# Performance work log

Measured on AMD Instinct MI355X. Metric: run time of the kernel, lower is better.

The kernel has to match this reference:

```python
import jax, jax.numpy as jnp
import numpy as np

N = 100000      # nodes
E = 3200000     # edges (avg degree 32)
F_IN = 128      # num_node_features
H = 128         # hidden_channels


def gcn_conv(x, edge_index, W, b, n):
    """PyG-style GCNConv: linear transform, add self-loops, symmetric
    D^{-1/2} A D^{-1/2} normalization, scatter-add aggregation, bias."""
    h = x @ W  # [n, out]
    row, col = edge_index[0], edge_index[1]
    loop = jnp.arange(n, dtype=row.dtype)
    row = jnp.concatenate([row, loop])
    col = jnp.concatenate([col, loop])
    deg = jax.ops.segment_sum(jnp.ones(row.shape, h.dtype), col, num_segments=n)
    dinv = jnp.where(deg > 0, jax.lax.rsqrt(deg), 0.0)
    norm = dinv[row] * dinv[col]                 # [E+n]
    msg = h[row] * norm[:, None]                 # gather + scale
    out = jax.ops.segment_sum(msg, col, num_segments=n)  # scatter-add
    return out + b


def setup_inputs() -> dict:
    key = jax.random.key(0)
    ks = jax.random.split(key, 8)
    x = jax.random.normal(ks[0], (N, F_IN), jnp.float32)
    edge_index = jax.random.randint(ks[1], (2, E), 0, N, dtype=jnp.int32)
    s1 = 1.0 / np.sqrt(F_IN)
    s2 = 1.0 / np.sqrt(H)
    W1 = jax.random.normal(ks[2], (F_IN, H), jnp.float32) * s1
    b1 = jnp.zeros((H,), jnp.float32)
    W2 = jax.random.normal(ks[3], (H, H), jnp.float32) * s2
    b2 = jnp.zeros((H,), jnp.float32)
    Wl = jax.random.normal(ks[4], (H, 1), jnp.float32) * s2
    bl = jnp.zeros((1,), jnp.float32)
    return {"x": x, "edge_index": edge_index, "W1": W1, "b1": b1,
            "W2": W2, "b2": b2, "Wl": Wl, "bl": bl}


def reference(x, edge_index, W1, b1, W2, b2, Wl, bl):
    n = x.shape[0]
    h = jax.nn.relu(gcn_conv(x, edge_index, W1, b1, n))
    # dropout p=0.5 is identity in eval mode (training=False)
    h = jax.nn.relu(gcn_conv(h, edge_index, W2, b2, n))
    return jax.nn.sigmoid(h @ Wl + bl)  # [n, 1]
```

## Files before the change

kernel.cpp:

```cpp
#include <hip/hip_runtime.h>
#include <math.h>

#define FDIM 128
#define BKT_BITS 8
#define BKT_W (1 << BKT_BITS)
#define BIN_CHUNK 6272

typedef short bf16x8 __attribute__((ext_vector_type(8)));
typedef float f32x4 __attribute__((ext_vector_type(4)));
typedef float f32x2 __attribute__((ext_vector_type(2)));

union ABu { bf16x8 v; unsigned int u[4]; };
union F4u { float4 f; float a[4]; };

__device__ inline unsigned int pack_bf16x2(float a, float b) {
  unsigned int ua = __float_as_uint(a);
  unsigned int ub = __float_as_uint(b);
  ua = (ua + 0x7fffu + ((ua >> 16) & 1u)) >> 16;
  ub = (ub + 0x7fffu + ((ub >> 16) & 1u)) >> 16;
  return ua | (ub << 16);
}

__device__ inline unsigned char f32_to_fp8(float v) {
  return (unsigned char)(__builtin_amdgcn_cvt_pk_fp8_f32(v, v, 0, false) & 0xff);
}


__global__ __launch_bounds__(256)
void k_bhist(const int* __restrict__ col, int* __restrict__ gbcnt, int nE, int nb) {
  __shared__ int lds[512];
  for (int i = threadIdx.x; i < 512; i += 256) lds[i] = 0;
  __syncthreads();
  int stride = gridDim.x * blockDim.x;
  for (int e = blockIdx.x * blockDim.x + threadIdx.x; e < nE; e += stride)
    atomicAdd(&lds[col[e] >> BKT_BITS], 1);
  __syncthreads();
  for (int b = threadIdx.x; b < nb; b += 256) {
    int c = lds[b];
    if (c) atomicAdd(&gbcnt[b], c);
  }
}

__global__ __launch_bounds__(512)
void k_bscan(const int* __restrict__ gbcnt, int* __restrict__ gboff,
             int* __restrict__ gcur, int nb, int nE) {
  __shared__ int lds[512];
  int t = threadIdx.x;
  lds[t] = (t < nb) ? gbcnt[t] : 0;
  __syncthreads();
  for (int off = 1; off < 512; off <<= 1) {
    int x = (t >= off) ? lds[t - off] : 0;
    __syncthreads();
    lds[t] += x;
    __syncthreads();
  }
  if (t < nb) {
    int excl = (t == 0) ? 0 : lds[t - 1];
    gboff[t] = excl;
    gcur[t] = excl;
  }
  if (t == 0) gboff[nb] = nE;
}

__global__ __launch_bounds__(256)
void k_bin(const int* __restrict__ row, const int* __restrict__ col,
           int* __restrict__ gcur, int* __restrict__ pairs, int nE, int chunk, int nb) {
  __shared__ int bcnt[512];
  __shared__ int lcur[512];
  __shared__ int ecol[BIN_CHUNK];
  int e0 = blockIdx.x * chunk;
  int e1 = min(e0 + chunk, nE);
  int m = e1 - e0;
  for (int i = threadIdx.x; i < 512; i += 256) bcnt[i] = 0;
  for (int i = threadIdx.x; i < m; i += 256) ecol[i] = col[e0 + i];
  __syncthreads();
  for (int i = threadIdx.x; i < m; i += 256)
    atomicAdd(&bcnt[((unsigned)ecol[i]) >> BKT_BITS], 1);
  __syncthreads();
  for (int b = threadIdx.x; b < nb; b += 256) {
    int c = bcnt[b];
    lcur[b] = c ? atomicAdd(&gcur[b], c) : 0;
  }
  __syncthreads();
  for (int i = threadIdx.x; i < m; i += 256) {
    int c = ecol[i];
    int r = row[e0 + i];
    int p = atomicAdd(&lcur[((unsigned)c) >> BKT_BITS], 1);
    pairs[p] = r | ((c & (BKT_W - 1)) << 24);
  }
}

__global__ __launch_bounds__(1024)
void k_fine(const int* __restrict__ pairs, const int* __restrict__ gboff,
            int* __restrict__ srcs, int* __restrict__ offs, int* __restrict__ cnt,
            float* __restrict__ dinv, int n) {
  __shared__ int lcnt[256];
  __shared__ int lcur[256];
  int b = blockIdx.x;
  int t = threadIdx.x;
  int ebase = gboff[b];
  int eend = gboff[b + 1];
  if (t < 256) lcnt[t] = 0;
  __syncthreads();
  for (int e = ebase + t; e < eend; e += 1024)
    atomicAdd(&lcnt[((unsigned)pairs[e]) >> 24], 1);
  __syncthreads();
  int orig = (t < 256) ? lcnt[t] : 0;
  for (int off = 1; off < 256; off <<= 1) {
    int x = (t < 256 && t >= off) ? lcnt[t - off] : 0;
    __syncthreads();
    if (t < 256) lcnt[t] += x;
    __syncthreads();
  }
  if (t < 256) {
    int excl = lcnt[t] - orig;
    int v = (b << BKT_BITS) + t;
    if (v < n) {
      offs[v] = ebase + excl;
      cnt[v] = orig;
      dinv[v] = rsqrtf((float)(orig + 1));
    }
    lcur[t] = ebase + excl;
  }
  __syncthreads();
  for (int e = ebase + t; e < eend; e += 1024) {
    int pr = pairs[e];
    int p = atomicAdd(&lcur[((unsigned)pr) >> 24], 1);
    srcs[p] = pr & 0x00FFFFFF;
  }
}

#define STAGE_WT()                                                          \
  {                                                                         \
    int c = threadIdx.x & 127;                                              \
    for (int kp = (threadIdx.x >> 7); kp < 64; kp += 2) {                   \
      float w0 = W[(kp * 2) * 128 + c];                                     \
      float w1 = W[(kp * 2 + 1) * 128 + c];                                 \
      int unit = kp >> 2, dw = kp & 3;                                      \
      wlds[c * 64 + ((unit ^ (c & 15)) << 2) + dw] = pack_bf16x2(w0, w1);   \
    }                                                                       \
  }                                                                         \
  __syncthreads();

#define GEMM_BODY()                                                         \
  int l = threadIdx.x & 63;                                                 \
  int grp = l >> 4, c15 = l & 15;                                           \
  int rbase = blockIdx.x * 64 + (threadIdx.x >> 6) * 16;                    \
  F4u dv;                                                                   \
  dv.f = *(const float4*)(dinv + rbase + grp * 4);                          \
  f32x4 acc[8];                                                             \
  _Pragma("unroll")                                                         \
  for (int nt = 0; nt < 8; ++nt) acc[nt] = (f32x4){0.f, 0.f, 0.f, 0.f};    \
  _Pragma("unroll")                                                         \
  for (int nt = 0; nt < 8; ++nt) {                                          \
    _Pragma("unroll")                                                       \
    for (int ks = 0; ks < 4; ++ks) {                                        \
      ABu b;                                                                \
      b.v = *(const bf16x8*)&wlds[(nt * 16 + c15) * 64 +                    \
                                  ((((ks << 2) + grp) ^ c15) << 2)];        \
      acc[nt] = __builtin_amdgcn_mfma_f32_16x16x32_bf16(a[ks].v, b.v,       \
                                                        acc[nt], 0, 0, 0);  \
    }                                                                       \
  }                                                                         \
  _Pragma("unroll")                                                         \
  for (int nt = 0; nt < 8; ++nt) {                                          \
    _Pragma("unroll")                                                       \
    for (int i = 0; i < 4; ++i) {                                           \
      int r = rbase + grp * 4 + i;                                          \
      if (r < n) {                                                          \
        float v = acc[nt][i] * dv.a[i];                                     \
        out[(size_t)r * 128 + nt * 16 + c15] = f32_to_fp8(v);               \
      }                                                                     \
    }                                                                       \
  }

__global__ __launch_bounds__(256)
void k_gemm_mfma_f(const float* __restrict__ in, const float* __restrict__ W,
                   const float* __restrict__ dinv, unsigned char* __restrict__ out,
                   int n) {
  __shared__ unsigned int wlds[128 * 64];
  STAGE_WT();
  {
    int l0 = threadIdx.x & 63;
    int row = blockIdx.x * 64 + (threadIdx.x >> 6) * 16 + (l0 & 15);
    int rowc = min(row, n - 1);
    int grp0 = l0 >> 4;
    const float4* xr = (const float4*)(in + (size_t)rowc * 128);
    ABu a[4];
#pragma unroll
    for (int ks = 0; ks < 4; ++ks) {
      float4 f0 = xr[ks * 8 + grp0 * 2];
      float4 f1 = xr[ks * 8 + grp0 * 2 + 1];
      a[ks].u[0] = pack_bf16x2(f0.x, f0.y);
      a[ks].u[1] = pack_bf16x2(f0.z, f0.w);
      a[ks].u[2] = pack_bf16x2(f1.x, f1.y);
      a[ks].u[3] = pack_bf16x2(f1.z, f1.w);
    }
    GEMM_BODY();
  }
}

__global__ __launch_bounds__(256)
void k_gemm_mfma_b(const unsigned int* __restrict__ in, const float* __restrict__ W,
                   const float* __restrict__ dinv, unsigned char* __restrict__ out,
                   int n) {
  __shared__ unsigned int wlds[128 * 64];
  STAGE_WT();
  {
    int l0 = threadIdx.x & 63;
    int row = blockIdx.x * 64 + (threadIdx.x >> 6) * 16 + (l0 & 15);
    int rowc = min(row, n - 1);
    int grp0 = l0 >> 4;
    const unsigned int* hr = in + (size_t)rowc * 64;
    ABu a[4];
#pragma unroll
    for (int ks = 0; ks < 4; ++ks)
      a[ks].v = *(const bf16x8*)&hr[ks * 16 + grp0 * 4];
    GEMM_BODY();
  }
}

__device__ inline float4 agg_core(const unsigned int* __restrict__ s4,
                                  const int* __restrict__ offs,
                                  const int* __restrict__ cnt,
                                  const int* __restrict__ srcs,
                                  int v, int lane) {
  int cl = lane & 31;
  int hf = lane >> 5;
  float4 acc = make_float4(0.f, 0.f, 0.f, 0.f);
  if (lane < 32) {
    unsigned int q = s4[(size_t)v * 32 + cl];
    f32x2 lo = __builtin_amdgcn_cvt_pk_f32_fp8((int)q, false);
    f32x2 hi = __builtin_amdgcn_cvt_pk_f32_fp8((int)q, true);
    acc = make_float4(lo[0], lo[1], hi[0], hi[1]);
  }
  int beg = offs[v];
  int m = cnt[v];
  for (int base = 0; base < m; base += 64) {
    int take = m - base;
    if (take > 64) take = 64;
    int idx = (lane < take) ? srcs[beg + base + lane] : 0;
    int it = 0;
    for (; it + 7 < take; it += 8) {
      int u0 = __shfl(idx, it + hf, 64);
      int u1 = __shfl(idx, it + 2 + hf, 64);
      int u2 = __shfl(idx, it + 4 + hf, 64);
      int u3 = __shfl(idx, it + 6 + hf, 64);
      unsigned int q0 = s4[(size_t)u0 * 32 + cl];
      unsigned int q1 = s4[(size_t)u1 * 32 + cl];
      unsigned int q2 = s4[(size_t)u2 * 32 + cl];
      unsigned int q3 = s4[(size_t)u3 * 32 + cl];
      f32x2 l0 = __builtin_amdgcn_cvt_pk_f32_fp8((int)q0, false);
      f32x2 h0 = __builtin_amdgcn_cvt_pk_f32_fp8((int)q0, true);
      f32x2 l1 = __builtin_amdgcn_cvt_pk_f32_fp8((int)q1, false);
      f32x2 h1 = __builtin_amdgcn_cvt_pk_f32_fp8((int)q1, true);
      f32x2 l2 = __builtin_amdgcn_cvt_pk_f32_fp8((int)q2, false);
      f32x2 h2 = __builtin_amdgcn_cvt_pk_f32_fp8((int)q2, true);
      f32x2 l3 = __builtin_amdgcn_cvt_pk_f32_fp8((int)q3, false);
      f32x2 h3 = __builtin_amdgcn_cvt_pk_f32_fp8((int)q3, true);
      acc.x += (l0[0] + l1[0]) + (l2[0] + l3[0]);
      acc.y += (l0[1] + l1[1]) + (l2[1] + l3[1]);
      acc.z += (h0[0] + h1[0]) + (h2[0] + h3[0]);
      acc.w += (h0[1] + h1[1]) + (h2[1] + h3[1]);
    }
    for (; it + 1 < take; it += 2) {
      int u = __shfl(idx, it + hf, 64);
      unsigned int q = s4[(size_t)u * 32 + cl];
      f32x2 lo = __builtin_amdgcn_cvt_pk_f32_fp8((int)q, false);
      f32x2 hi = __builtin_amdgcn_cvt_pk_f32_fp8((int)q, true);
      acc.x += lo[0]; acc.y += lo[1]; acc.z += hi[0]; acc.w += hi[1];
    }
    if (it < take) {
      int u = __shfl(idx, it, 64);
      if (lane < 32) {
        unsigned int q = s4[(size_t)u * 32 + cl];
        f32x2 lo = __builtin_amdgcn_cvt_pk_f32_fp8((int)q, false);
        f32x2 hi = __builtin_amdgcn_cvt_pk_f32_fp8((int)q, true);
        acc.x += lo[0]; acc.y += lo[1]; acc.z += hi[0]; acc.w += hi[1];
      }
    }
  }
  acc.x += __shfl_xor(acc.x, 32, 64);
  acc.y += __shfl_xor(acc.y, 32, 64);
  acc.z += __shfl_xor(acc.z, 32, 64);
  acc.w += __shfl_xor(acc.w, 32, 64);
  return acc;
}

__global__ __launch_bounds__(256)
void k_agg_mid(const unsigned int* __restrict__ s4, const int* __restrict__ offs,
               const int* __restrict__ cnt, const int* __restrict__ srcs,
               const float* __restrict__ dinv, const float* __restrict__ bias,
               unsigned int* __restrict__ hb, int n) {
  int v = (int)(((size_t)blockIdx.x * blockDim.x + threadIdx.x) >> 6);
  if (v >= n) return;
  int lane = threadIdx.x & 63;
  float4 acc = agg_core(s4, offs, cnt, srcs, v, lane);
  if (lane < 32) {
    int cl = lane;
    float d = dinv[v];
    float4 bb = ((const float4*)bias)[cl];
    float r0 = fmaxf(acc.x * d + bb.x, 0.0f);
    float r1 = fmaxf(acc.y * d + bb.y, 0.0f);
    float r2 = fmaxf(acc.z * d + bb.z, 0.0f);
    float r3 = fmaxf(acc.w * d + bb.w, 0.0f);
    uint2 pk;
    pk.x = pack_bf16x2(r0, r1);
    pk.y = pack_bf16x2(r2, r3);
    ((uint2*)hb)[(size_t)v * 32 + cl] = pk;
  }
}

__global__ __launch_bounds__(256)
void k_agg_head(const unsigned int* __restrict__ s4, const int* __restrict__ offs,
                const int* __restrict__ cnt, const int* __restrict__ srcs,
                const float* __restrict__ dinv, const float* __restrict__ bias,
                const float* __restrict__ Wl, const float* __restrict__ bl,
                float* __restrict__ out, int n) {
  int v = (int)(((size_t)blockIdx.x * blockDim.x + threadIdx.x) >> 6);
  if (v >= n) return;
  int lane = threadIdx.x & 63;
  float4 acc = agg_core(s4, offs, cnt, srcs, v, lane);
  float p = 0.0f;
  if (lane < 32) {
    int cl = lane;
    float d = dinv[v];
    float4 bb = ((const float4*)bias)[cl];
    float4 wv = ((const float4*)Wl)[cl];
    float r0 = fmaxf(acc.x * d + bb.x, 0.0f);
    float r1 = fmaxf(acc.y * d + bb.y, 0.0f);
    float r2 = fmaxf(acc.z * d + bb.z, 0.0f);
    float r3 = fmaxf(acc.w * d + bb.w, 0.0f);
    p = r0 * wv.x + r1 * wv.y + r2 * wv.z + r3 * wv.w;
  }
  p += __shfl_down(p, 16, 64);
  p += __shfl_down(p, 8, 64);
  p += __shfl_down(p, 4, 64);
  p += __shfl_down(p, 2, 64);
  p += __shfl_down(p, 1, 64);
  if (lane == 0) {
    float z = p + bl[0];
    out[v] = 1.0f / (1.0f + expf(-z));
  }
}


extern "C" void kernel_launch(void* const* d_in, const int* in_sizes, int n_in,
                              void* d_out, int out_size, void* d_ws, size_t ws_size,
                              hipStream_t stream) {
  const float* x  = (const float*)d_in[0];
  const int*   ei = (const int*)d_in[1];
  const float* W1 = (const float*)d_in[2];
  const float* b1 = (const float*)d_in[3];
  const float* W2 = (const float*)d_in[4];
  const float* b2 = (const float*)d_in[5];
  const float* Wl = (const float*)d_in[6];
  const float* bl = (const float*)d_in[7];
  float* out = (float*)d_out;

  int n  = in_sizes[0] / FDIM;
  int nE = in_sizes[1] / 2;
  const int* row = ei;
  const int* col = ei + nE;
  int nb = (n + BKT_W - 1) >> BKT_BITS;

  unsigned char* s8 = (unsigned char*)d_ws;
  unsigned int* hb  = (unsigned int*)(s8 + (size_t)n * 128);
  float* dinv  = (float*)(hb + (size_t)n * 64);
  int*   cnt   = (int*)(dinv + n);
  int*   offs  = cnt + n;
  int*   srcs  = offs + n;
  int*   gbcnt = srcs + nE;
  int*   gboff = gbcnt + nb;
  int*   gcur  = gboff + nb + 1;
  int*   pairs = (int*)hb;

  hipMemsetAsync(gbcnt, 0, (size_t)nb * sizeof(int), stream);
  k_bhist<<<1024, 256, 0, stream>>>(col, gbcnt, nE, nb);
  k_bscan<<<1, 512, 0, stream>>>(gbcnt, gboff, gcur, nb, nE);
  int chunk = (nE + 511) / 512;
  k_bin<<<512, 256, 0, stream>>>(row, col, gcur, pairs, nE, chunk, nb);
  k_fine<<<nb, 1024, 0, stream>>>(pairs, gboff, srcs, offs, cnt, dinv, n);

  int gemm_grid = (n + 63) / 64;
  int wave_grid = (n + 3) / 4;
  k_gemm_mfma_f<<<gemm_grid, 256, 0, stream>>>(x, W1, dinv, s8, n);
  k_agg_mid<<<wave_grid, 256, 0, stream>>>((const unsigned int*)s8, offs, cnt, srcs, dinv, b1, hb, n);
  k_gemm_mfma_b<<<gemm_grid, 256, 0, stream>>>(hb, W2, dinv, s8, n);
  k_agg_head<<<wave_grid, 256, 0, stream>>>((const unsigned int*)s8, offs, cnt, srcs, dinv, b2, Wl, bl, out, n);
}
```

Baseline: 375.1 us.

## Persistent GEMM grid, wider gather unroll, and smaller binning launches

```diff
diff --git a/kernel.cpp b/kernel.cpp
--- a/kernel.cpp
+++ b/kernel.cpp
@@ -4,7 +4,7 @@
 #define FDIM 128
 #define BKT_BITS 8
 #define BKT_W (1 << BKT_BITS)
-#define BIN_CHUNK 6272
+#define BIN_CHUNK 12544
 
 typedef short bf16x8 __attribute__((ext_vector_type(8)));
 typedef float f32x4 __attribute__((ext_vector_type(4)));
@@ -90,7 +90,7 @@
   }
 }
 
-__global__ __launch_bounds__(1024)
+__global__ __launch_bounds__(256)
 void k_fine(const int* __restrict__ pairs, const int* __restrict__ gboff,
             int* __restrict__ srcs, int* __restrict__ offs, int* __restrict__ cnt,
             float* __restrict__ dinv, int n) {
@@ -100,30 +100,28 @@
   int t = threadIdx.x;
   int ebase = gboff[b];
   int eend = gboff[b + 1];
-  if (t < 256) lcnt[t] = 0;
-  __syncthreads();
-  for (int e = ebase + t; e < eend; e += 1024)
+  lcnt[t] = 0;
+  __syncthreads();
+  for (int e = ebase + t; e < eend; e += 256)
     atomicAdd(&lcnt[((unsigned)pairs[e]) >> 24], 1);
   __syncthreads();
-  int orig = (t < 256) ? lcnt[t] : 0;
+  int orig = lcnt[t];
   for (int off = 1; off < 256; off <<= 1) {
-    int x = (t < 256 && t >= off) ? lcnt[t - off] : 0;
+    int x = (t >= off) ? lcnt[t - off] : 0;
     __syncthreads();
-    if (t < 256) lcnt[t] += x;
+    lcnt[t] += x;
     __syncthreads();
   }
-  if (t < 256) {
-    int excl = lcnt[t] - orig;
-    int v = (b << BKT_BITS) + t;
-    if (v < n) {
-      offs[v] = ebase + excl;
-      cnt[v] = orig;
-      dinv[v] = rsqrtf((float)(orig + 1));
-    }
-    lcur[t] = ebase + excl;
-  }
-  __syncthreads();
-  for (int e = ebase + t; e < eend; e += 1024) {
+  int excl = lcnt[t] - orig;
+  int v = (b << BKT_BITS) + t;
+  if (v < n) {
+    offs[v] = ebase + excl;
+    cnt[v] = orig;
+    dinv[v] = rsqrtf((float)(orig + 1));
+  }
+  lcur[t] = ebase + excl;
+  __syncthreads();
+  for (int e = ebase + t; e < eend; e += 256) {
     int pr = pairs[e];
     int p = atomicAdd(&lcur[((unsigned)pr) >> 24], 1);
     srcs[p] = pr & 0x00FFFFFF;
@@ -142,81 +140,82 @@
   }                                                                         \
   __syncthreads();
 
-#define GEMM_BODY()                                                         \
-  int l = threadIdx.x & 63;                                                 \
-  int grp = l >> 4, c15 = l & 15;                                           \
-  int rbase = blockIdx.x * 64 + (threadIdx.x >> 6) * 16;                    \
-  F4u dv;                                                                   \
-  dv.f = *(const float4*)(dinv + rbase + grp * 4);                          \
-  f32x4 acc[8];                                                             \
-  _Pragma("unroll")                                                         \
-  for (int nt = 0; nt < 8; ++nt) acc[nt] = (f32x4){0.f, 0.f, 0.f, 0.f};    \
-  _Pragma("unroll")                                                         \
-  for (int nt = 0; nt < 8; ++nt) {                                          \
+#define GEMM_TILE()                                                         \
+  {                                                                         \
+    F4u dv;                                                                 \
+    dv.f = *(const float4*)(dinv + rbase + grp * 4);                        \
+    f32x4 acc[8];                                                           \
     _Pragma("unroll")                                                       \
-    for (int ks = 0; ks < 4; ++ks) {                                        \
-      ABu b;                                                                \
-      b.v = *(const bf16x8*)&wlds[(nt * 16 + c15) * 64 +                    \
-                                  ((((ks << 2) + grp) ^ c15) << 2)];        \
-      acc[nt] = __builtin_amdgcn_mfma_f32_16x16x32_bf16(a[ks].v, b.v,       \
-                                                        acc[nt], 0, 0, 0);  \
-    }                                                                       \
-  }                                                                         \
-  _Pragma("unroll")                                                         \
-  for (int nt = 0; nt < 8; ++nt) {                                          \
+    for (int nt = 0; nt < 8; ++nt) acc[nt] = (f32x4){0.f, 0.f, 0.f, 0.f};   \
     _Pragma("unroll")                                                       \
-    for (int i = 0; i < 4; ++i) {                                           \
-      int r = rbase + grp * 4 + i;                                          \
-      if (r < n) {                                                          \
-        float v = acc[nt][i] * dv.a[i];                                     \
-        out[(size_t)r * 128 + nt * 16 + c15] = f32_to_fp8(v);               \
+    for (int nt = 0; nt < 8; ++nt) {                                        \
+      _Pragma("unroll")                                                     \
+      for (int ks = 0; ks < 4; ++ks) {                                      \
+        ABu b;                                                              \
+        b.v = *(const bf16x8*)&wlds[(nt * 16 + c15) * 64 +                  \
+                                    ((((ks << 2) + grp) ^ c15) << 2)];      \
+        acc[nt] = __builtin_amdgcn_mfma_f32_16x16x32_bf16(a[ks].v, b.v,     \
+                                                          acc[nt], 0, 0, 0);\
       }                                                                     \
     }                                                                       \
+    _Pragma("unroll")                                                       \
+    for (int nt = 0; nt < 8; ++nt) {                                        \
+      _Pragma("unroll")                                                     \
+      for (int i = 0; i < 4; ++i) {                                         \
+        int r = rbase + grp * 4 + i;                                        \
+        if (r < n) {                                                        \
+          float v = acc[nt][i] * dv.a[i];                                   \
+          out[(size_t)r * 128 + nt * 16 + c15] = f32_to_fp8(v);             \
+        }                                                                   \
+      }                                                                     \
+    }                                                                       \
   }
 
 __global__ __launch_bounds__(256)
 void k_gemm_mfma_f(const float* __restrict__ in, const float* __restrict__ W,
                    const float* __restrict__ dinv, unsigned char* __restrict__ out,
-                   int n) {
+                   int n, int ntiles) {
   __shared__ unsigned int wlds[128 * 64];
   STAGE_WT();
-  {
-    int l0 = threadIdx.x & 63;
-    int row = blockIdx.x * 64 + (threadIdx.x >> 6) * 16 + (l0 & 15);
-    int rowc = min(row, n - 1);
-    int grp0 = l0 >> 4;
+  int l = threadIdx.x & 63;
+  int wv = threadIdx.x >> 6;
+  int grp = l >> 4, c15 = l & 15;
+  for (int tile = blockIdx.x; tile < ntiles; tile += gridDim.x) {
+    int rbase = tile * 64 + wv * 16;
+    int rowc = min(rbase + c15, n - 1);
     const float4* xr = (const float4*)(in + (size_t)rowc * 128);
     ABu a[4];
 #pragma unroll
     for (int ks = 0; ks < 4; ++ks) {
-      float4 f0 = xr[ks * 8 + grp0 * 2];
-      float4 f1 = xr[ks * 8 + grp0 * 2 + 1];
+      float4 f0 = xr[ks * 8 + grp * 2];
+      float4 f1 = xr[ks * 8 + grp * 2 + 1];
       a[ks].u[0] = pack_bf16x2(f0.x, f0.y);
       a[ks].u[1] = pack_bf16x2(f0.z, f0.w);
       a[ks].u[2] = pack_bf16x2(f1.x, f1.y);
       a[ks].u[3] = pack_bf16x2(f1.z, f1.w);
     }
-    GEMM_BODY();
+    GEMM_TILE();
   }
 }
 
 __global__ __launch_bounds__(256)
 void k_gemm_mfma_b(const unsigned int* __restrict__ in, const float* __restrict__ W,
                    const float* __restrict__ dinv, unsigned char* __restrict__ out,
-                   int n) {
+                   int n, int ntiles) {
   __shared__ unsigned int wlds[128 * 64];
   STAGE_WT();
-  {
-    int l0 = threadIdx.x & 63;
-    int row = blockIdx.x * 64 + (threadIdx.x >> 6) * 16 + (l0 & 15);
-    int rowc = min(row, n - 1);
-    int grp0 = l0 >> 4;
+  int l = threadIdx.x & 63;
+  int wv = threadIdx.x >> 6;
+  int grp = l >> 4, c15 = l & 15;
+  for (int tile = blockIdx.x; tile < ntiles; tile += gridDim.x) {
+    int rbase = tile * 64 + wv * 16;
+    int rowc = min(rbase + c15, n - 1);
     const unsigned int* hr = in + (size_t)rowc * 64;
     ABu a[4];
 #pragma unroll
     for (int ks = 0; ks < 4; ++ks)
-      a[ks].v = *(const bf16x8*)&hr[ks * 16 + grp0 * 4];
-    GEMM_BODY();
+      a[ks].v = *(const bf16x8*)&hr[ks * 16 + grp * 4];
+    GEMM_TILE();
   }
 }
 
@@ -241,15 +240,23 @@
     if (take > 64) take = 64;
     int idx = (lane < take) ? srcs[beg + base + lane] : 0;
     int it = 0;
-    for (; it + 7 < take; it += 8) {
+    for (; it + 15 < take; it += 16) {
       int u0 = __shfl(idx, it + hf, 64);
       int u1 = __shfl(idx, it + 2 + hf, 64);
       int u2 = __shfl(idx, it + 4 + hf, 64);
       int u3 = __shfl(idx, it + 6 + hf, 64);
+      int u4 = __shfl(idx, it + 8 + hf, 64);
+      int u5 = __shfl(idx, it + 10 + hf, 64);
+      int u6 = __shfl(idx, it + 12 + hf, 64);
+      int u7 = __shfl(idx, it + 14 + hf, 64);
       unsigned int q0 = s4[(size_t)u0 * 32 + cl];
       unsigned int q1 = s4[(size_t)u1 * 32 + cl];
       unsigned int q2 = s4[(size_t)u2 * 32 + cl];
       unsigned int q3 = s4[(size_t)u3 * 32 + cl];
+      unsigned int q4 = s4[(size_t)u4 * 32 + cl];
+      unsigned int q5 = s4[(size_t)u5 * 32 + cl];
+      unsigned int q6 = s4[(size_t)u6 * 32 + cl];
+      unsigned int q7 = s4[(size_t)u7 * 32 + cl];
       f32x2 l0 = __builtin_amdgcn_cvt_pk_f32_fp8((int)q0, false);
       f32x2 h0 = __builtin_amdgcn_cvt_pk_f32_fp8((int)q0, true);
       f32x2 l1 = __builtin_amdgcn_cvt_pk_f32_fp8((int)q1, false);
@@ -258,10 +265,18 @@
       f32x2 h2 = __builtin_amdgcn_cvt_pk_f32_fp8((int)q2, true);
       f32x2 l3 = __builtin_amdgcn_cvt_pk_f32_fp8((int)q3, false);
       f32x2 h3 = __builtin_amdgcn_cvt_pk_f32_fp8((int)q3, true);
-      acc.x += (l0[0] + l1[0]) + (l2[0] + l3[0]);
-      acc.y += (l0[1] + l1[1]) + (l2[1] + l3[1]);
-      acc.z += (h0[0] + h1[0]) + (h2[0] + h3[0]);
-      acc.w += (h0[1] + h1[1]) + (h2[1] + h3[1]);
+      f32x2 l4 = __builtin_amdgcn_cvt_pk_f32_fp8((int)q4, false);
+      f32x2 h4 = __builtin_amdgcn_cvt_pk_f32_fp8((int)q4, true);
+      f32x2 l5 = __builtin_amdgcn_cvt_pk_f32_fp8((int)q5, false);
+      f32x2 h5 = __builtin_amdgcn_cvt_pk_f32_fp8((int)q5, true);
+      f32x2 l6 = __builtin_amdgcn_cvt_pk_f32_fp8((int)q6, false);
+      f32x2 h6 = __builtin_amdgcn_cvt_pk_f32_fp8((int)q6, true);
+      f32x2 l7 = __builtin_amdgcn_cvt_pk_f32_fp8((int)q7, false);
+      f32x2 h7 = __builtin_amdgcn_cvt_pk_f32_fp8((int)q7, true);
+      acc.x += ((l0[0] + l1[0]) + (l2[0] + l3[0])) + ((l4[0] + l5[0]) + (l6[0] + l7[0]));
+      acc.y += ((l0[1] + l1[1]) + (l2[1] + l3[1])) + ((l4[1] + l5[1]) + (l6[1] + l7[1]));
+      acc.z += ((h0[0] + h1[0]) + (h2[0] + h3[0])) + ((h4[0] + h5[0]) + (h6[0] + h7[0]));
+      acc.w += ((h0[1] + h1[1]) + (h2[1] + h3[1])) + ((h4[1] + h5[1]) + (h6[1] + h7[1]));
     }
     for (; it + 1 < take; it += 2) {
       int u = __shfl(idx, it + hf, 64);
@@ -376,16 +391,16 @@
   int*   pairs = (int*)hb;
 
   hipMemsetAsync(gbcnt, 0, (size_t)nb * sizeof(int), stream);
-  k_bhist<<<1024, 256, 0, stream>>>(col, gbcnt, nE, nb);
+  k_bhist<<<256, 256, 0, stream>>>(col, gbcnt, nE, nb);
   k_bscan<<<1, 512, 0, stream>>>(gbcnt, gboff, gcur, nb, nE);
-  int chunk = (nE + 511) / 512;
-  k_bin<<<512, 256, 0, stream>>>(row, col, gcur, pairs, nE, chunk, nb);
-  k_fine<<<nb, 1024, 0, stream>>>(pairs, gboff, srcs, offs, cnt, dinv, n);
-
-  int gemm_grid = (n + 63) / 64;
+  int chunk = (nE + 255) / 256;
+  k_bin<<<256, 256, 0, stream>>>(row, col, gcur, pairs, nE, chunk, nb);
+  k_fine<<<nb, 256, 0, stream>>>(pairs, gboff, srcs, offs, cnt, dinv, n);
+
+  int ntiles = (n + 63) / 64;
   int wave_grid = (n + 3) / 4;
-  k_gemm_mfma_f<<<gemm_grid, 256, 0, stream>>>(x, W1, dinv, s8, n);
+  k_gemm_mfma_f<<<512, 256, 0, stream>>>(x, W1, dinv, s8, n, ntiles);
   k_agg_mid<<<wave_grid, 256, 0, stream>>>((const unsigned int*)s8, offs, cnt, srcs, dinv, b1, hb, n);
-  k_gemm_mfma_b<<<gemm_grid, 256, 0, stream>>>(hb, W2, dinv, s8, n);
+  k_gemm_mfma_b<<<512, 256, 0, stream>>>(hb, W2, dinv, s8, n, ntiles);
   k_agg_head<<<wave_grid, 256, 0, stream>>>((const unsigned int*)s8, offs, cnt, srcs, dinv, b2, Wl, bl, out, n);
 }
```

New measurement: 382.2 us. Within noise of the previous version (+1.9%).

## Prescale CSR source offsets, load neighbor indices directly, and retune CSR-build launches

Applied to the files above, without the earlier changes.

```diff
diff --git a/kernel.cpp b/kernel.cpp
--- a/kernel.cpp
+++ b/kernel.cpp
@@ -4,7 +4,7 @@
 #define FDIM 128
 #define BKT_BITS 8
 #define BKT_W (1 << BKT_BITS)
-#define BIN_CHUNK 6272
+#define BIN_CHUNK 12544
 
 typedef short bf16x8 __attribute__((ext_vector_type(8)));
 typedef float f32x4 __attribute__((ext_vector_type(4)));
@@ -90,7 +90,7 @@
   }
 }
 
-__global__ __launch_bounds__(1024)
+__global__ __launch_bounds__(256)
 void k_fine(const int* __restrict__ pairs, const int* __restrict__ gboff,
             int* __restrict__ srcs, int* __restrict__ offs, int* __restrict__ cnt,
             float* __restrict__ dinv, int n) {
@@ -100,33 +100,31 @@
   int t = threadIdx.x;
   int ebase = gboff[b];
   int eend = gboff[b + 1];
-  if (t < 256) lcnt[t] = 0;
-  __syncthreads();
-  for (int e = ebase + t; e < eend; e += 1024)
+  lcnt[t] = 0;
+  __syncthreads();
+  for (int e = ebase + t; e < eend; e += 256)
     atomicAdd(&lcnt[((unsigned)pairs[e]) >> 24], 1);
   __syncthreads();
-  int orig = (t < 256) ? lcnt[t] : 0;
+  int orig = lcnt[t];
   for (int off = 1; off < 256; off <<= 1) {
-    int x = (t < 256 && t >= off) ? lcnt[t - off] : 0;
+    int x = (t >= off) ? lcnt[t - off] : 0;
     __syncthreads();
-    if (t < 256) lcnt[t] += x;
+    lcnt[t] += x;
     __syncthreads();
   }
-  if (t < 256) {
-    int excl = lcnt[t] - orig;
-    int v = (b << BKT_BITS) + t;
-    if (v < n) {
-      offs[v] = ebase + excl;
-      cnt[v] = orig;
-      dinv[v] = rsqrtf((float)(orig + 1));
-    }
-    lcur[t] = ebase + excl;
-  }
-  __syncthreads();
-  for (int e = ebase + t; e < eend; e += 1024) {
+  int excl = lcnt[t] - orig;
+  int v = (b << BKT_BITS) + t;
+  if (v < n) {
+    offs[v] = ebase + excl;
+    cnt[v] = orig;
+    dinv[v] = rsqrtf((float)(orig + 1));
+  }
+  lcur[t] = ebase + excl;
+  __syncthreads();
+  for (int e = ebase + t; e < eend; e += 256) {
     int pr = pairs[e];
     int p = atomicAdd(&lcur[((unsigned)pr) >> 24], 1);
-    srcs[p] = pr & 0x00FFFFFF;
+    srcs[p] = (pr & 0x00FFFFFF) << 7;
   }
 }
 
@@ -220,65 +218,75 @@
   }
 }
 
-__device__ inline float4 agg_core(const unsigned int* __restrict__ s4,
+__device__ inline float4 agg_core(const unsigned char* __restrict__ s8,
                                   const int* __restrict__ offs,
                                   const int* __restrict__ cnt,
                                   const int* __restrict__ srcs,
                                   int v, int lane) {
   int cl = lane & 31;
   int hf = lane >> 5;
+  int co = cl * 4;
   float4 acc = make_float4(0.f, 0.f, 0.f, 0.f);
   if (lane < 32) {
-    unsigned int q = s4[(size_t)v * 32 + cl];
+    unsigned int q = *(const unsigned int*)(s8 + (unsigned)(v * 128 + co));
     f32x2 lo = __builtin_amdgcn_cvt_pk_f32_fp8((int)q, false);
     f32x2 hi = __builtin_amdgcn_cvt_pk_f32_fp8((int)q, true);
     acc = make_float4(lo[0], lo[1], hi[0], hi[1]);
   }
-  int beg = offs[v];
   int m = cnt[v];
-  for (int base = 0; base < m; base += 64) {
-    int take = m - base;
-    if (take > 64) take = 64;
-    int idx = (lane < take) ? srcs[beg + base + lane] : 0;
-    int it = 0;
-    for (; it + 7 < take; it += 8) {
-      int u0 = __shfl(idx, it + hf, 64);
-      int u1 = __shfl(idx, it + 2 + hf, 64);
-      int u2 = __shfl(idx, it + 4 + hf, 64);
-      int u3 = __shfl(idx, it + 6 + hf, 64);
-      unsigned int q0 = s4[(size_t)u0 * 32 + cl];
-      unsigned int q1 = s4[(size_t)u1 * 32 + cl];
-      unsigned int q2 = s4[(size_t)u2 * 32 + cl];
-      unsigned int q3 = s4[(size_t)u3 * 32 + cl];
-      f32x2 l0 = __builtin_amdgcn_cvt_pk_f32_fp8((int)q0, false);
-      f32x2 h0 = __builtin_amdgcn_cvt_pk_f32_fp8((int)q0, true);
-      f32x2 l1 = __builtin_amdgcn_cvt_pk_f32_fp8((int)q1, false);
-      f32x2 h1 = __builtin_amdgcn_cvt_pk_f32_fp8((int)q1, true);
-      f32x2 l2 = __builtin_amdgcn_cvt_pk_f32_fp8((int)q2, false);
-      f32x2 h2 = __builtin_amdgcn_cvt_pk_f32_fp8((int)q2, true);
-      f32x2 l3 = __builtin_amdgcn_cvt_pk_f32_fp8((int)q3, false);
-      f32x2 h3 = __builtin_amdgcn_cvt_pk_f32_fp8((int)q3, true);
-      acc.x += (l0[0] + l1[0]) + (l2[0] + l3[0]);
-      acc.y += (l0[1] + l1[1]) + (l2[1] + l3[1]);
-      acc.z += (h0[0] + h1[0]) + (h2[0] + h3[0]);
-      acc.w += (h0[1] + h1[1]) + (h2[1] + h3[1]);
-    }
-    for (; it + 1 < take; it += 2) {
-      int u = __shfl(idx, it + hf, 64);
-      unsigned int q = s4[(size_t)u * 32 + cl];
-      f32x2 lo = __builtin_amdgcn_cvt_pk_f32_fp8((int)q, false);
-      f32x2 hi = __builtin_amdgcn_cvt_pk_f32_fp8((int)q, true);
-      acc.x += lo[0]; acc.y += lo[1]; acc.z += hi[0]; acc.w += hi[1];
-    }
-    if (it < take) {
-      int u = __shfl(idx, it, 64);
-      if (lane < 32) {
-        unsigned int q = s4[(size_t)u * 32 + cl];
-        f32x2 lo = __builtin_amdgcn_cvt_pk_f32_fp8((int)q, false);
-        f32x2 hi = __builtin_amdgcn_cvt_pk_f32_fp8((int)q, true);
-        acc.x += lo[0]; acc.y += lo[1]; acc.z += hi[0]; acc.w += hi[1];
-      }
-    }
+  const int* sp = srcs + offs[v];
+  int it = 0;
+  for (; it + 15 < m; it += 16) {
+    int o0 = sp[it + hf];
+    int o1 = sp[it + 2 + hf];
+    int o2 = sp[it + 4 + hf];
+    int o3 = sp[it + 6 + hf];
+    int o4 = sp[it + 8 + hf];
+    int o5 = sp[it + 10 + hf];
+    int o6 = sp[it + 12 + hf];
+    int o7 = sp[it + 14 + hf];
+    unsigned int q0 = *(const unsigned int*)(s8 + (unsigned)(o0 + co));
+    unsigned int q1 = *(const unsigned int*)(s8 + (unsigned)(o1 + co));
+    unsigned int q2 = *(const unsigned int*)(s8 + (unsigned)(o2 + co));
+    unsigned int q3 = *(const unsigned int*)(s8 + (unsigned)(o3 + co));
+    unsigned int q4 = *(const unsigned int*)(s8 + (unsigned)(o4 + co));
+    unsigned int q5 = *(const unsigned int*)(s8 + (unsigned)(o5 + co));
+    unsigned int q6 = *(const unsigned int*)(s8 + (unsigned)(o6 + co));
+    unsigned int q7 = *(const unsigned int*)(s8 + (unsigned)(o7 + co));
+    f32x2 l0 = __builtin_amdgcn_cvt_pk_f32_fp8((int)q0, false);
+    f32x2 h0 = __builtin_amdgcn_cvt_pk_f32_fp8((int)q0, true);
+    f32x2 l1 = __builtin_amdgcn_cvt_pk_f32_fp8((int)q1, false);
+    f32x2 h1 = __builtin_amdgcn_cvt_pk_f32_fp8((int)q1, true);
+    f32x2 l2 = __builtin_amdgcn_cvt_pk_f32_fp8((int)q2, false);
+    f32x2 h2 = __builtin_amdgcn_cvt_pk_f32_fp8((int)q2, true);
+    f32x2 l3 = __builtin_amdgcn_cvt_pk_f32_fp8((int)q3, false);
+    f32x2 h3 = __builtin_amdgcn_cvt_pk_f32_fp8((int)q3, true);
+    f32x2 l4 = __builtin_amdgcn_cvt_pk_f32_fp8((int)q4, false);
+    f32x2 h4 = __builtin_amdgcn_cvt_pk_f32_fp8((int)q4, true);
+    f32x2 l5 = __builtin_amdgcn_cvt_pk_f32_fp8((int)q5, false);
+    f32x2 h5 = __builtin_amdgcn_cvt_pk_f32_fp8((int)q5, true);
+    f32x2 l6 = __builtin_amdgcn_cvt_pk_f32_fp8((int)q6, false);
+    f32x2 h6 = __builtin_amdgcn_cvt_pk_f32_fp8((int)q6, true);
+    f32x2 l7 = __builtin_amdgcn_cvt_pk_f32_fp8((int)q7, false);
+    f32x2 h7 = __builtin_amdgcn_cvt_pk_f32_fp8((int)q7, true);
+    acc.x += ((l0[0] + l1[0]) + (l2[0] + l3[0])) + ((l4[0] + l5[0]) + (l6[0] + l7[0]));
+    acc.y += ((l0[1] + l1[1]) + (l2[1] + l3[1])) + ((l4[1] + l5[1]) + (l6[1] + l7[1]));
+    acc.z += ((h0[0] + h1[0]) + (h2[0] + h3[0])) + ((h4[0] + h5[0]) + (h6[0] + h7[0]));
+    acc.w += ((h0[1] + h1[1]) + (h2[1] + h3[1])) + ((h4[1] + h5[1]) + (h6[1] + h7[1]));
+  }
+  for (; it + 1 < m; it += 2) {
+    int o = sp[it + hf];
+    unsigned int q = *(const unsigned int*)(s8 + (unsigned)(o + co));
+    f32x2 lo = __builtin_amdgcn_cvt_pk_f32_fp8((int)q, false);
+    f32x2 hi = __builtin_amdgcn_cvt_pk_f32_fp8((int)q, true);
+    acc.x += lo[0]; acc.y += lo[1]; acc.z += hi[0]; acc.w += hi[1];
+  }
+  if (it < m && lane < 32) {
+    int o = sp[it];
+    unsigned int q = *(const unsigned int*)(s8 + (unsigned)(o + co));
+    f32x2 lo = __builtin_amdgcn_cvt_pk_f32_fp8((int)q, false);
+    f32x2 hi = __builtin_amdgcn_cvt_pk_f32_fp8((int)q, true);
+    acc.x += lo[0]; acc.y += lo[1]; acc.z += hi[0]; acc.w += hi[1];
   }
   acc.x += __shfl_xor(acc.x, 32, 64);
   acc.y += __shfl_xor(acc.y, 32, 64);
@@ -288,14 +296,14 @@
 }
 
 __global__ __launch_bounds__(256)
-void k_agg_mid(const unsigned int* __restrict__ s4, const int* __restrict__ offs,
+void k_agg_mid(const unsigned char* __restrict__ s8, const int* __restrict__ offs,
                const int* __restrict__ cnt, const int* __restrict__ srcs,
                const float* __restrict__ dinv, const float* __restrict__ bias,
                unsigned int* __restrict__ hb, int n) {
   int v = (int)(((size_t)blockIdx.x * blockDim.x + threadIdx.x) >> 6);
   if (v >= n) return;
   int lane = threadIdx.x & 63;
-  float4 acc = agg_core(s4, offs, cnt, srcs, v, lane);
+  float4 acc = agg_core(s8, offs, cnt, srcs, v, lane);
   if (lane < 32) {
     int cl = lane;
     float d = dinv[v];
@@ -312,7 +320,7 @@
 }
 
 __global__ __launch_bounds__(256)
-void k_agg_head(const unsigned int* __restrict__ s4, const int* __restrict__ offs,
+void k_agg_head(const unsigned char* __restrict__ s8, const int* __restrict__ offs,
                 const int* __restrict__ cnt, const int* __restrict__ srcs,
                 const float* __restrict__ dinv, const float* __restrict__ bias,
                 const float* __restrict__ Wl, const float* __restrict__ bl,
@@ -320,7 +328,7 @@
   int v = (int)(((size_t)blockIdx.x * blockDim.x + threadIdx.x) >> 6);
   if (v >= n) return;
   int lane = threadIdx.x & 63;
-  float4 acc = agg_core(s4, offs, cnt, srcs, v, lane);
+  float4 acc = agg_core(s8, offs, cnt, srcs, v, lane);
   float p = 0.0f;
   if (lane < 32) {
     int cl = lane;
@@ -376,16 +384,16 @@
   int*   pairs = (int*)hb;
 
   hipMemsetAsync(gbcnt, 0, (size_t)nb * sizeof(int), stream);
-  k_bhist<<<1024, 256, 0, stream>>>(col, gbcnt, nE, nb);
+  k_bhist<<<256, 256, 0, stream>>>(col, gbcnt, nE, nb);
   k_bscan<<<1, 512, 0, stream>>>(gbcnt, gboff, gcur, nb, nE);
-  int chunk = (nE + 511) / 512;
-  k_bin<<<512, 256, 0, stream>>>(row, col, gcur, pairs, nE, chunk, nb);
-  k_fine<<<nb, 1024, 0, stream>>>(pairs, gboff, srcs, offs, cnt, dinv, n);
+  int chunk = (nE + 255) / 256;
+  k_bin<<<256, 256, 0, stream>>>(row, col, gcur, pairs, nE, chunk, nb);
+  k_fine<<<nb, 256, 0, stream>>>(pairs, gboff, srcs, offs, cnt, dinv, n);
 
   int gemm_grid = (n + 63) / 64;
   int wave_grid = (n + 3) / 4;
   k_gemm_mfma_f<<<gemm_grid, 256, 0, stream>>>(x, W1, dinv, s8, n);
-  k_agg_mid<<<wave_grid, 256, 0, stream>>>((const unsigned int*)s8, offs, cnt, srcs, dinv, b1, hb, n);
+  k_agg_mid<<<wave_grid, 256, 0, stream>>>(s8, offs, cnt, srcs, dinv, b1, hb, n);
   k_gemm_mfma_b<<<gemm_grid, 256, 0, stream>>>(hb, W2, dinv, s8, n);
-  k_agg_head<<<wave_grid, 256, 0, stream>>>((const unsigned int*)s8, offs, cnt, srcs, dinv, b2, Wl, bl, out, n);
-}
+  k_agg_head<<<wave_grid, 256, 0, stream>>>(s8, offs, cnt, srcs, dinv, b2, Wl, bl, out, n);
+}
```

New measurement: 392.2 us. +4.6%, slower.
